# Optimization experiments

Hardware: AMD Instinct MI355X
Metric: run time of the kernel (lower is better)

The kernel has to match this reference:

```python
import jax, jax.numpy as jnp
import numpy as np

B, T, C, NH, RD = 128, 512, 384, 6, 16
HD = C // NH
SEQ_LEN = 512


def setup_inputs() -> dict:
    key = jax.random.key(0)
    kx, kqkv, kout = jax.random.split(key, 3)
    x = jax.random.normal(kx, (B, T, C), dtype=jnp.float32)
    # torch nn.Linear weights are [out_features, in_features]
    Wqkv = jax.random.normal(kqkv, (3 * C, C), dtype=jnp.float32) * 0.02
    Wout = jax.random.normal(kout, (C, C), dtype=jnp.float32) * 0.02
    freqs = 1.0 / (10000.0 ** (jnp.arange(0, RD, 2, dtype=jnp.float32) / RD))  # [RD//2]
    f = jnp.outer(jnp.arange(SEQ_LEN, dtype=jnp.float32), freqs)  # [SEQ_LEN, RD//2]
    cos = jnp.cos(f)[None, None]  # [1,1,SEQ_LEN,RD//2]
    sin = jnp.sin(f)[None, None]
    return {"x": x, "Wqkv": Wqkv, "Wout": Wout, "cos": cos, "sin": sin}


def _rope(t, c, s, rd):
    # t: [B, NH, T, HD]; partial rotary on first rd channels
    r, p = t[..., :rd], t[..., rd:]
    r1, r2 = r[..., : rd // 2], r[..., rd // 2:]
    rot = jnp.concatenate([r1 * c - r2 * s, r2 * c + r1 * s], axis=-1)
    return jnp.concatenate([rot, p], axis=-1)


def reference(x, Wqkv, Wout, cos, sin):
    b, t, c = x.shape
    nh, hd, rd = NH, c // NH, RD
    qkv = jnp.einsum("btc,dc->btd", x, Wqkv).reshape(b, t, 3, nh, hd)
    q, k, v = (jnp.transpose(qkv[:, :, i], (0, 2, 1, 3)) for i in range(3))  # [b,nh,t,hd]
    cc = cos[:, :, :t]
    ss = sin[:, :, :t]
    q = _rope(q, cc, ss, rd)
    k = _rope(k, cc, ss, rd)
    scale = 1.0 / jnp.sqrt(jnp.asarray(hd, dtype=x.dtype))
    scores = jnp.einsum("bhqd,bhkd->bhqk", q, k) * scale
    causal = jnp.tril(jnp.ones((t, t), dtype=bool))
    scores = jnp.where(causal, scores, jnp.finfo(scores.dtype).min)
    att = jax.nn.softmax(scores, axis=-1)
    o = jnp.einsum("bhqk,bhkd->bhqd", att, v)  # [b,nh,t,hd]
    o = jnp.transpose(o, (0, 2, 1, 3)).reshape(b, t, c)
    return jnp.einsum("btc,dc->btd", o, Wout)
```

## Files before the change

kernel.cpp:

```cpp
#include <hip/hip_runtime.h>

#define B_DIM 128
#define T_DIM 512
#define C_DIM 384
#define NH_DIM 6
#define HD_DIM 64
#define QKV_LD 1152

typedef __bf16 bf16x8 __attribute__((ext_vector_type(8)));
typedef __bf16 bf16x4 __attribute__((ext_vector_type(4)));
typedef float f32x4 __attribute__((ext_vector_type(4)));

__device__ __forceinline__ void gload_lds16(const __bf16* g, __bf16* l) {
  __builtin_amdgcn_global_load_lds(
      (const __attribute__((address_space(1))) void*)g,
      (__attribute__((address_space(3))) void*)l, 16, 0, 0);
}

#define X_F4 6291456
#define WQKV_F4 110592
#define WOUT_F4 36864
__global__ __launch_bounds__(256) void cast_all(const float* __restrict__ x,
                                                const float* __restrict__ wqkv,
                                                const float* __restrict__ wout,
                                                __bf16* __restrict__ xb,
                                                __bf16* __restrict__ wqkvb,
                                                __bf16* __restrict__ woutb) {
  int i = blockIdx.x * blockDim.x + threadIdx.x;
  const float4* src;
  bf16x4* dst;
  if (i < X_F4) {
    src = (const float4*)x + i;
    dst = (bf16x4*)xb + i;
  } else if (i < X_F4 + WQKV_F4) {
    src = (const float4*)wqkv + (i - X_F4);
    dst = (bf16x4*)wqkvb + (i - X_F4);
  } else {
    src = (const float4*)wout + (i - X_F4 - WQKV_F4);
    dst = (bf16x4*)woutb + (i - X_F4 - WQKV_F4);
  }
  float4 v = *src;
  bf16x4 o;
  o[0] = (__bf16)v.x; o[1] = (__bf16)v.y; o[2] = (__bf16)v.z; o[3] = (__bf16)v.w;
  *dst = o;
}

__global__ __launch_bounds__(256) void gemm_bt(const __bf16* __restrict__ A,
                                               const __bf16* __restrict__ Bm,
                                               __bf16* __restrict__ Cb,
                                               float* __restrict__ Cf,
                                               const float* __restrict__ cosp,
                                               const float* __restrict__ sinp,
                                               int M, int N, int K) {
  __shared__ __attribute__((aligned(16))) __bf16 As[128 * 32];
  __shared__ __attribute__((aligned(16))) __bf16 Bs[128 * 32];
  const int m0 = blockIdx.y * 128;
  const int n0 = blockIdx.x * 128;
  const int tid = threadIdx.x;
  const int wave = tid >> 6;
  const int lane = tid & 63;
  const int lr = lane & 15;
  const int quad = lane >> 4;
  const int wm = (wave & 1) * 64;
  const int wn = (wave >> 1) * 64;
  const int ca0 = wave * 2, ca1 = wave * 2 + 1;
  const int srow = lane >> 2;
  const int row0 = ca0 * 16 + srow, row1 = ca1 * 16 + srow;
  const int slot = (lane & 3) ^ ((lane >> 3) & 3);
  const int rs = (quad ^ ((lr >> 1) & 3)) * 8;
  f32x4 acc[4][4] = {};
  for (int k0 = 0; k0 < K; k0 += 32) {
    __syncthreads();
    gload_lds16(&A[(size_t)(m0 + row0) * K + k0 + slot * 8], &As[ca0 * 512]);
    gload_lds16(&A[(size_t)(m0 + row1) * K + k0 + slot * 8], &As[ca1 * 512]);
    gload_lds16(&Bm[(size_t)(n0 + row0) * K + k0 + slot * 8], &Bs[ca0 * 512]);
    gload_lds16(&Bm[(size_t)(n0 + row1) * K + k0 + slot * 8], &Bs[ca1 * 512]);
    __syncthreads();
    bf16x8 af[4], bf[4];
#pragma unroll
    for (int i = 0; i < 4; ++i)
      af[i] = *(bf16x8*)&As[(wm + i * 16 + lr) * 32 + rs];
#pragma unroll
    for (int j = 0; j < 4; ++j)
      bf[j] = *(bf16x8*)&Bs[(wn + j * 16 + lr) * 32 + rs];
#pragma unroll
    for (int i = 0; i < 4; ++i)
#pragma unroll
      for (int j = 0; j < 4; ++j)
        acc[i][j] = __builtin_amdgcn_mfma_f32_16x16x32_bf16(af[i], bf[j], acc[i][j], 0, 0, 0);
  }
  const bool doRope = (cosp != nullptr);
#pragma unroll
  for (int i = 0; i < 4; ++i) {
#pragma unroll
    for (int j = 0; j < 4; ++j) {
      int gm = m0 + wm + i * 16 + quad * 4;
      int gn = n0 + wn + j * 16 + lr;
      if (Cf) {
#pragma unroll
        for (int r = 0; r < 4; ++r) Cf[(size_t)(gm + r) * N + gn] = acc[i][j][r];
      } else {
        const int cbase = n0 + wn + j * 16;
        const bool ropeBlk = doRope && (cbase < 2 * C_DIM) && ((cbase & 63) == 0);
        if (ropeBlk) {
#pragma unroll
          for (int r = 0; r < 4; ++r) {
            float v = acc[i][j][r];
            float p = __shfl_xor(v, 8, 64);
            int t = (gm + r) & (T_DIM - 1);
            float c = cosp[t * 8 + (lr & 7)];
            float s = sinp[t * 8 + (lr & 7)];
            v = (lr & 8) ? __builtin_fmaf(v, c, p * s)
                         : __builtin_fmaf(v, c, -p * s);
            Cb[(size_t)(gm + r) * N + gn] = (__bf16)v;
          }
        } else {
#pragma unroll
          for (int r = 0; r < 4; ++r) Cb[(size_t)(gm + r) * N + gn] = (__bf16)acc[i][j][r];
        }
      }
    }
  }
}

__global__ __launch_bounds__(256) void transpose_v(const __bf16* __restrict__ qkv,
                                                   __bf16* __restrict__ vt) {
  __shared__ __attribute__((aligned(16))) __bf16 Tl[64][72];
  const int tt = blockIdx.x;
  const int h = blockIdx.y;
  const int b = blockIdx.z;
  const int tid = threadIdx.x;
  const __bf16* src = qkv + (size_t)b * T_DIM * QKV_LD + 2 * C_DIM + h * HD_DIM;
#pragma unroll
  for (int i = 0; i < 2; ++i) {
    int c = tid + i * 256;
    int row = c >> 3, cc = (c & 7) * 8;
    *(bf16x8*)&Tl[row][cc] = *(const bf16x8*)&src[(size_t)(tt * 64 + row) * QKV_LD + cc];
  }
  __syncthreads();
  __bf16* dst = vt + (size_t)(b * NH_DIM + h) * HD_DIM * T_DIM + tt * 64;
#pragma unroll
  for (int i = 0; i < 2; ++i) {
    int c = tid + i * 256;
    int drow = c >> 3, tc = (c & 7) * 8;
    bf16x8 v;
#pragma unroll
    for (int j = 0; j < 8; ++j) v[j] = Tl[tc + j][drow];
    *(bf16x8*)&dst[(size_t)drow * T_DIM + tc] = v;
  }
}

__global__ __launch_bounds__(256) void attn_kernel(const __bf16* __restrict__ qkv,
                                                   const __bf16* __restrict__ vt,
                                                   __bf16* __restrict__ o) {
  __shared__ __attribute__((aligned(16))) __bf16 K0s[64 * 64];
  __shared__ __attribute__((aligned(16))) __bf16 K1s[64 * 64];
  __shared__ __attribute__((aligned(16))) __bf16 V0s[64 * 64];
  __shared__ __attribute__((aligned(16))) __bf16 V1s[64 * 64];
  __shared__ __attribute__((aligned(16))) __bf16 Pl[4][16][72];
  const int qt = blockIdx.x;
  const int h = blockIdx.y;
  const int b = blockIdx.z;
  const int tid = threadIdx.x;
  const int wave = tid >> 6;
  const int lane = tid & 63;
  const int lr = lane & 15;
  const int quad = lane >> 4;
  const __bf16* qbase = qkv + (size_t)b * T_DIM * QKV_LD + h * HD_DIM;
  const __bf16* kbase = qbase + C_DIM;
  const __bf16* vtb = vt + (size_t)(b * NH_DIM + h) * HD_DIM * T_DIM;
  const int qrow0 = qt * 64 + wave * 16;
  const int myq = qrow0 + lr;
  bf16x8 qf[2];
#pragma unroll
  for (int ks = 0; ks < 2; ++ks)
    qf[ks] = *(const bf16x8*)&qbase[(size_t)(qrow0 + lr) * QKV_LD + ks * 32 + quad * 8];
  f32x4 oacc[4] = {};
  float m_i = -3.0e38f, l_i = 0.f;
  const float kScale = 0.18033688011112042f;
  const int gsl = ((lane & 7) ^ ((lane >> 3) & 7)) * 8;
  const int grA = wave * 8 + (lane >> 3);
  const int grB = grA + 32;
  const int ldsA = wave * 512;
  const int ldsB = (wave + 4) * 512;
  auto stage = [&](int kt, __bf16* KT, __bf16* VT) {
    const __bf16* ks = kbase + (size_t)(kt * 64) * QKV_LD;
    const __bf16* vs = vtb + kt * 64;
    gload_lds16(&ks[(size_t)grA * QKV_LD + gsl], KT + ldsA);
    gload_lds16(&ks[(size_t)grB * QKV_LD + gsl], KT + ldsB);
    gload_lds16(&vs[(size_t)grA * T_DIM + gsl], VT + ldsA);
    gload_lds16(&vs[(size_t)grB * T_DIM + gsl], VT + ldsB);
  };
  const int sw0 = ((quad ^ (lr & 7)) * 8);
  const int sw1 = (((4 + quad) ^ (lr & 7)) * 8);
  auto body = [&](const __bf16* KT, const __bf16* VT, int kt) {
    f32x4 sj[4];
#pragma unroll
    for (int j = 0; j < 4; ++j) {
      f32x4 z = {};
      bf16x8 kf0 = *(const bf16x8*)&KT[(j * 16 + lr) * 64 + sw0];
      bf16x8 kf1 = *(const bf16x8*)&KT[(j * 16 + lr) * 64 + sw1];
      z = __builtin_amdgcn_mfma_f32_16x16x32_bf16(kf0, qf[0], z, 0, 0, 0);
      z = __builtin_amdgcn_mfma_f32_16x16x32_bf16(kf1, qf[1], z, 0, 0, 0);
      sj[j] = z;
    }
    float mloc = -3.0e38f;
#pragma unroll
    for (int j = 0; j < 4; ++j)
#pragma unroll
      for (int r = 0; r < 4; ++r) {
        if (kt == qt) {
          int key = kt * 64 + j * 16 + quad * 4 + r;
          if (key > myq) sj[j][r] = -3.0e38f;
        }
        mloc = fmaxf(mloc, sj[j][r]);
      }
    mloc = fmaxf(mloc, __shfl_xor(mloc, 16, 64));
    mloc = fmaxf(mloc, __shfl_xor(mloc, 32, 64));
    mloc *= kScale;
    if (__any(mloc - m_i > 8.0f)) {
      float mn = fmaxf(m_i, mloc);
      float a = exp2f(m_i - mn);
      m_i = mn;
      l_i *= a;
      float ar[4];
#pragma unroll
      for (int r = 0; r < 4; ++r) ar[r] = __shfl(a, quad * 4 + r, 64);
#pragma unroll
      for (int dt = 0; dt < 4; ++dt)
#pragma unroll
        for (int r = 0; r < 4; ++r) oacc[dt][r] *= ar[r];
    }
    float rsum = 0.f;
#pragma unroll
    for (int j = 0; j < 4; ++j) {
      bf16x4 pw;
#pragma unroll
      for (int r = 0; r < 4; ++r) {
        float p = exp2f(__builtin_fmaf(sj[j][r], kScale, -m_i));
        rsum += p;
        pw[r] = (__bf16)p;
      }
      *(bf16x4*)&Pl[wave][lr][j * 16 + quad * 4] = pw;
    }
    rsum += __shfl_xor(rsum, 16, 64);
    rsum += __shfl_xor(rsum, 32, 64);
    l_i += rsum;
    bf16x8 pf[2];
#pragma unroll
    for (int ks = 0; ks < 2; ++ks)
      pf[ks] = *(bf16x8*)&Pl[wave][lr][ks * 32 + quad * 8];
#pragma unroll
    for (int dt = 0; dt < 4; ++dt) {
      bf16x8 vf0 = *(const bf16x8*)&VT[(dt * 16 + lr) * 64 + sw0];
      bf16x8 vf1 = *(const bf16x8*)&VT[(dt * 16 + lr) * 64 + sw1];
      oacc[dt] = __builtin_amdgcn_mfma_f32_16x16x32_bf16(pf[0], vf0, oacc[dt], 0, 0, 0);
      oacc[dt] = __builtin_amdgcn_mfma_f32_16x16x32_bf16(pf[1], vf1, oacc[dt], 0, 0, 0);
    }
  };
  stage(0, K0s, V0s);
  __syncthreads();
  int kt = 0;
  while (true) {
    if (kt < qt) stage(kt + 1, K1s, V1s);
    body(K0s, V0s, kt);
    __syncthreads();
    ++kt;
    if (kt > qt) break;
    if (kt < qt) stage(kt + 1, K0s, V0s);
    body(K1s, V1s, kt);
    __syncthreads();
    ++kt;
    if (kt > qt) break;
  }
  float linv = 1.f / l_i;
  float lrow[4];
#pragma unroll
  for (int r = 0; r < 4; ++r) lrow[r] = __shfl(linv, quad * 4 + r, 64);
#pragma unroll
  for (int dt = 0; dt < 4; ++dt)
#pragma unroll
    for (int r = 0; r < 4; ++r) {
      size_t row = (size_t)b * T_DIM + qrow0 + quad * 4 + r;
      o[row * C_DIM + h * HD_DIM + dt * 16 + lr] = (__bf16)(oacc[dt][r] * lrow[r]);
    }
}

extern "C" void kernel_launch(void* const* d_in, const int* in_sizes, int n_in,
                              void* d_out, int out_size, void* d_ws, size_t ws_size,
                              hipStream_t stream) {
  const float* x    = (const float*)d_in[0];
  const float* wqkv = (const float*)d_in[1];
  const float* wout = (const float*)d_in[2];
  const float* cosp = (const float*)d_in[3];
  const float* sinp = (const float*)d_in[4];
  float* out = (float*)d_out;

  char* ws = (char*)d_ws;
  __bf16* xb    = (__bf16*)(ws);
  __bf16* wqkvb = (__bf16*)(ws + 50331648);
  __bf16* woutb = (__bf16*)(ws + 51216384);
  __bf16* qkvb  = (__bf16*)(ws + 51511296);
  __bf16* ob    = (__bf16*)(ws + 202506240);
  __bf16* vtb   = xb;

  const int M = B_DIM * T_DIM;

  cast_all<<<25152, 256, 0, stream>>>(x, wqkv, wout, xb, wqkvb, woutb);

  gemm_bt<<<dim3(QKV_LD / 128, M / 128), 256, 0, stream>>>(
      xb, wqkvb, qkvb, (float*)nullptr, cosp, sinp, M, QKV_LD, C_DIM);

  transpose_v<<<dim3(T_DIM / 64, NH_DIM, B_DIM), 256, 0, stream>>>(qkvb, vtb);

  attn_kernel<<<dim3(T_DIM / 64, NH_DIM, B_DIM), 256, 0, stream>>>(qkvb, vtb, ob);

  gemm_bt<<<dim3(C_DIM / 128, M / 128), 256, 0, stream>>>(
      ob, woutb, (__bf16*)nullptr, out, (const float*)nullptr, (const float*)nullptr,
      M, C_DIM, C_DIM);
}
```

Baseline: 462.6 us.

## Keep attention P in registers by permuting key order in S MFMA

Reorders which K rows each MFMA j-tile reads so the S accumulator layout matches the A-operand layout of the PV MFMA. P can then be packed into bf16x8 registers directly, with no round trip through the per-wave LDS buffer. The LDS swizzle keys for K and V change to stay bank-conflict free under the new row access pattern, and the causal mask key index is remapped to match. This removes an LDS write and read plus its latency from every key tile, at the cost of more intricate index math that must stay consistent with the swizzle.

```diff
diff --git a/kernel.cpp b/kernel.cpp
--- a/kernel.cpp
+++ b/kernel.cpp
@@ -157,7 +157,6 @@
   __shared__ __attribute__((aligned(16))) __bf16 K1s[64 * 64];
   __shared__ __attribute__((aligned(16))) __bf16 V0s[64 * 64];
   __shared__ __attribute__((aligned(16))) __bf16 V1s[64 * 64];
-  __shared__ __attribute__((aligned(16))) __bf16 Pl[4][16][72];
   const int qt = blockIdx.x;
   const int h = blockIdx.y;
   const int b = blockIdx.z;
@@ -178,7 +177,8 @@
   f32x4 oacc[4] = {};
   float m_i = -3.0e38f, l_i = 0.f;
   const float kScale = 0.18033688011112042f;
-  const int gsl = ((lane & 7) ^ ((lane >> 3) & 7)) * 8;
+  const int skey = (((lane >> 3) & 3) << 1) | (wave & 1);
+  const int gsl = ((lane & 7) ^ skey) * 8;
   const int grA = wave * 8 + (lane >> 3);
   const int grB = grA + 32;
   const int ldsA = wave * 512;
@@ -191,15 +191,19 @@
     gload_lds16(&vs[(size_t)grA * T_DIM + gsl], VT + ldsA);
     gload_lds16(&vs[(size_t)grB * T_DIM + gsl], VT + ldsB);
   };
-  const int sw0 = ((quad ^ (lr & 7)) * 8);
-  const int sw1 = (((4 + quad) ^ (lr & 7)) * 8);
+  const int keyK = ((lr & 3) << 1) | ((lr >> 2) & 1);
+  const int keyV = ((lr & 3) << 1) | ((lr >> 3) & 1);
+  const int swK0 = (quad ^ keyK) * 8, swK1 = ((4 + quad) ^ keyK) * 8;
+  const int swV0 = (quad ^ keyV) * 8, swV1 = ((4 + quad) ^ keyV) * 8;
+  const int rkbase = ((lr >> 2) & 3) * 8 + (lr & 3);
   auto body = [&](const __bf16* KT, const __bf16* VT, int kt) {
     f32x4 sj[4];
 #pragma unroll
     for (int j = 0; j < 4; ++j) {
+      const int rK = (j >> 1) * 32 + (j & 1) * 4 + rkbase;
+      bf16x8 kf0 = *(const bf16x8*)&KT[rK * 64 + swK0];
+      bf16x8 kf1 = *(const bf16x8*)&KT[rK * 64 + swK1];
       f32x4 z = {};
-      bf16x8 kf0 = *(const bf16x8*)&KT[(j * 16 + lr) * 64 + sw0];
-      bf16x8 kf1 = *(const bf16x8*)&KT[(j * 16 + lr) * 64 + sw1];
       z = __builtin_amdgcn_mfma_f32_16x16x32_bf16(kf0, qf[0], z, 0, 0, 0);
       z = __builtin_amdgcn_mfma_f32_16x16x32_bf16(kf1, qf[1], z, 0, 0, 0);
       sj[j] = z;
@@ -210,7 +214,7 @@
 #pragma unroll
       for (int r = 0; r < 4; ++r) {
         if (kt == qt) {
-          int key = kt * 64 + j * 16 + quad * 4 + r;
+          int key = kt * 64 + (j >> 1) * 32 + quad * 8 + (j & 1) * 4 + r;
           if (key > myq) sj[j][r] = -3.0e38f;
         }
         mloc = fmaxf(mloc, sj[j][r]);
@@ -232,30 +236,25 @@
         for (int r = 0; r < 4; ++r) oacc[dt][r] *= ar[r];
     }
     float rsum = 0.f;
-#pragma unroll
-    for (int j = 0; j < 4; ++j) {
-      bf16x4 pw;
+    bf16x8 pf0, pf1;
+#pragma unroll
+    for (int j = 0; j < 4; ++j)
 #pragma unroll
       for (int r = 0; r < 4; ++r) {
-        float p = exp2f(__builtin_fmaf(sj[j][r], kScale, -m_i));
-        rsum += p;
-        pw[r] = (__bf16)p;
+        float pv = exp2f(__builtin_fmaf(sj[j][r], kScale, -m_i));
+        rsum += pv;
+        const int jj = (j & 1) * 4 + r;
+        if (j < 2) pf0[jj] = (__bf16)pv; else pf1[jj] = (__bf16)pv;
       }
-      *(bf16x4*)&Pl[wave][lr][j * 16 + quad * 4] = pw;
-    }
     rsum += __shfl_xor(rsum, 16, 64);
     rsum += __shfl_xor(rsum, 32, 64);
     l_i += rsum;
-    bf16x8 pf[2];
-#pragma unroll
-    for (int ks = 0; ks < 2; ++ks)
-      pf[ks] = *(bf16x8*)&Pl[wave][lr][ks * 32 + quad * 8];
 #pragma unroll
     for (int dt = 0; dt < 4; ++dt) {
-      bf16x8 vf0 = *(const bf16x8*)&VT[(dt * 16 + lr) * 64 + sw0];
-      bf16x8 vf1 = *(const bf16x8*)&VT[(dt * 16 + lr) * 64 + sw1];
-      oacc[dt] = __builtin_amdgcn_mfma_f32_16x16x32_bf16(pf[0], vf0, oacc[dt], 0, 0, 0);
-      oacc[dt] = __builtin_amdgcn_mfma_f32_16x16x32_bf16(pf[1], vf1, oacc[dt], 0, 0, 0);
+      bf16x8 vf0 = *(const bf16x8*)&VT[(dt * 16 + lr) * 64 + swV0];
+      bf16x8 vf1 = *(const bf16x8*)&VT[(dt * 16 + lr) * 64 + swV1];
+      oacc[dt] = __builtin_amdgcn_mfma_f32_16x16x32_bf16(pf0, vf0, oacc[dt], 0, 0, 0);
+      oacc[dt] = __builtin_amdgcn_mfma_f32_16x16x32_bf16(pf1, vf1, oacc[dt], 0, 0, 0);
     }
   };
   stage(0, K0s, V0s);
```

Measured after the change: 456.8 us. About the same (-1.3%).
